# Kernel tuning notes

Measured on AMD Instinct MI355X. Metric: run time of the kernel, lower is better.

Reference implementation:

```python
import jax, jax.numpy as jnp
import numpy as np

H, W = 256, 256
L = 1024
R = 4
B = 64
EPS = 1e-4
FF = (H + W) * R * 4


def setup_inputs() -> dict:
    key = jax.random.key(0)
    ks = jax.random.split(key, 8)
    x = jax.random.normal(ks[0], (B, L), dtype=jnp.float32)
    # Linear weights (torch Linear: out = x @ W.T), kaiming-uniform-ish init
    lim = 1.0 / np.sqrt(L)
    W_t = jax.random.uniform(ks[1], (FF, L), minval=-lim, maxval=lim, dtype=jnp.float32)
    W_g = jax.random.uniform(ks[2], (FF, L), minval=-lim, maxval=lim, dtype=jnp.float32)
    # weights_static: [2, H, W, 2]
    k_lim = np.sqrt(6.0 / (H * W))
    ws0 = jax.random.uniform(ks[3], (1, H, W, 2), minval=-k_lim, maxval=k_lim, dtype=jnp.float32)
    ws1_re = jax.random.uniform(ks[4], (1, H, W, 1), minval=EPS - 1.0, maxval=1.0 - EPS, dtype=jnp.float32)
    ws1_im = jax.random.uniform(ks[5], (1, H, W, 1), minval=-EPS, maxval=EPS, dtype=jnp.float32)
    weights_static = jnp.concatenate([ws0, jnp.concatenate([ws1_re, ws1_im], axis=-1)], axis=0)
    x_lim = np.sqrt(6.0 / (H + W))
    weights_mod = jax.random.uniform(ks[6], (4, H, W), minval=-x_lim, maxval=x_lim, dtype=jnp.float32)
    c_lim = 1.0 / np.sqrt(R)
    kc1, kc2 = jax.random.split(ks[7])
    conv_w = jax.random.uniform(kc1, (R, R), minval=-c_lim, maxval=c_lim, dtype=jnp.float32)  # [out_ch, in_ch] for 1x1 conv
    conv_b = jax.random.uniform(kc2, (R,), minval=-c_lim, maxval=c_lim, dtype=jnp.float32)
    return {"x": x, "W_t": W_t, "W_g": W_g, "weights_static": weights_static,
            "weights_mod": weights_mod, "conv_w": conv_w, "conv_b": conv_b}


def reference(x, W_t, W_g, weights_static, weights_mod, conv_w, conv_b):
    b = x.shape[0]
    xt = x @ W_t.T                                  # [B, FF]
    xg = x @ W_g.T
    xg = xg * jax.nn.sigmoid(xg)                    # SiLU-style gate
    mod = xt * xg
    mod = mod.reshape(b, 4, -1)
    mod = mod / jnp.sqrt(jnp.mean(jnp.abs(mod), axis=-1, keepdims=True) + EPS)
    mod = mod.reshape(b, 4, R, H + W)
    a_part = mod[..., :H]                           # [B,4,R,H]
    b_part = mod[..., H:]                           # [B,4,R,W]
    outer = jnp.einsum('bkri,bkrj->bkrij', a_part, b_part)  # [B,4,R,H,W]
    # 1x1 conv (R->R) followed by sum over output channels collapses to a
    # single contraction with column-summed weights + summed bias (same math).
    w_eff = conv_w.sum(axis=0)                      # [R]
    b_eff = conv_b.sum()
    mod = jnp.einsum('bkrij,r->bkij', outer, w_eff) + b_eff  # [B,4,H,W]
    mod = weights_mod[None] * mod
    A0 = weights_static[0]                          # [H,W,2]
    A1 = weights_static[1]                          # [H,W,2]
    Bc = jnp.moveaxis(mod[:, 0:2], 1, -1)           # [B,H,W,2]
    re = A1[..., 0] * Bc[..., 0] - A1[..., 1] * Bc[..., 1]
    im = A1[..., 0] * Bc[..., 1] - A1[..., 1] * Bc[..., 0]
    mag = jnp.sqrt(re * re + im * im + EPS)         # [B,H,W]
    mag = jnp.sqrt(jnp.mean(mag, axis=(-1, -2)) + EPS)  # [B]
    inv = 1.0 / mag[:, None, None]
    mw_re = A0[..., 0] + re * inv                   # [B,H,W]
    mw_im = A0[..., 1] + im * inv
    proj = jnp.moveaxis(mod[:, 2:4], 1, -1)         # [B,H,W,2]
    den = jnp.sqrt(proj[..., 0] ** 2 + proj[..., 1] ** 2 + EPS)
    theta_cos = proj[..., 0] / den
    theta_sin = proj[..., 1] / den
    return mw_re * theta_cos + mw_im * theta_sin    # [B,H,W]
```

## Files before the change

kernel.cpp:

```cpp
#include <hip/hip_runtime.h>

typedef __bf16 bf16x8 __attribute__((ext_vector_type(8)));
typedef float floatx4 __attribute__((ext_vector_type(4)));

__device__ inline void cvt8_hl(const float* __restrict__ p, bf16x8& h, bf16x8& l){
  float4 v0 = *reinterpret_cast<const float4*>(p);
  float4 v1 = *reinterpret_cast<const float4*>(p + 4);
  float v[8] = {v0.x, v0.y, v0.z, v0.w, v1.x, v1.y, v1.z, v1.w};
  #pragma unroll
  for (int i = 0; i < 8; ++i) {
    __bf16 hi = (__bf16)v[i];
    h[i] = hi;
    l[i] = (__bf16)(v[i] - (float)hi);
  }
}

__global__ __launch_bounds__(256) void k1_gemm(
    const float* __restrict__ x,
    const float* __restrict__ Wt,
    const float* __restrict__ Wg,
    float* __restrict__ mod)
{
  __shared__ float red[3][32][64];
  const int tid  = threadIdx.x;
  const int wave = tid >> 6, lane = tid & 63;
  const int quad = lane >> 4, r16 = lane & 15;
  const int ff = blockIdx.x * 16 + r16;
  const int kb = wave * 256 + quad * 8;

  floatx4 accT[4], accG[4];
  #pragma unroll
  for (int m = 0; m < 4; ++m) { accT[m] = (floatx4)0.0f; accG[m] = (floatx4)0.0f; }

  const float* wt = Wt + ff * 1024 + kb;
  const float* wg = Wg + ff * 1024 + kb;
  const float* xp = x  + r16 * 1024 + kb;

  #pragma unroll
  for (int it = 0; it < 8; ++it) {
    const int ko = it * 32;
    bf16x8 bth, btl, bgh, bgl;
    cvt8_hl(wt + ko, bth, btl);
    cvt8_hl(wg + ko, bgh, bgl);
    #pragma unroll
    for (int mt = 0; mt < 4; ++mt) {
      bf16x8 ah, al;
      cvt8_hl(xp + mt * 16384 + ko, ah, al);
      accT[mt] = __builtin_amdgcn_mfma_f32_16x16x32_bf16(ah, bth, accT[mt], 0, 0, 0);
      accT[mt] = __builtin_amdgcn_mfma_f32_16x16x32_bf16(ah, btl, accT[mt], 0, 0, 0);
      accT[mt] = __builtin_amdgcn_mfma_f32_16x16x32_bf16(al, bth, accT[mt], 0, 0, 0);
      accG[mt] = __builtin_amdgcn_mfma_f32_16x16x32_bf16(ah, bgh, accG[mt], 0, 0, 0);
      accG[mt] = __builtin_amdgcn_mfma_f32_16x16x32_bf16(ah, bgl, accG[mt], 0, 0, 0);
      accG[mt] = __builtin_amdgcn_mfma_f32_16x16x32_bf16(al, bgh, accG[mt], 0, 0, 0);
    }
  }

  if (wave != 0) {
    #pragma unroll
    for (int mt = 0; mt < 4; ++mt)
      #pragma unroll
      for (int r = 0; r < 4; ++r) {
        red[wave - 1][mt * 4 + r][lane]      = accT[mt][r];
        red[wave - 1][16 + mt * 4 + r][lane] = accG[mt][r];
      }
  }
  __syncthreads();
  if (wave == 0) {
    #pragma unroll
    for (int mt = 0; mt < 4; ++mt) {
      #pragma unroll
      for (int r = 0; r < 4; ++r) {
        float t = accT[mt][r] + red[0][mt * 4 + r][lane]
                              + red[1][mt * 4 + r][lane]
                              + red[2][mt * 4 + r][lane];
        float g = accG[mt][r] + red[0][16 + mt * 4 + r][lane]
                              + red[1][16 + mt * 4 + r][lane]
                              + red[2][16 + mt * 4 + r][lane];
        float sig = 1.0f / (1.0f + __expf(-g));
        int b = mt * 16 + quad * 4 + r;
        mod[b * 8192 + ff] = t * g * sig;
      }
    }
  }
}

__global__ __launch_bounds__(256) void k1b_scale(const float* __restrict__ mod,
                                                 float* __restrict__ s)
{
  const int row = blockIdx.x;
  const int tid = threadIdx.x;
  const float* p = mod + row * 2048;
  float sum = 0.0f;
  #pragma unroll
  for (int q = 0; q < 8; ++q) sum += fabsf(p[q * 256 + tid]);
  #pragma unroll
  for (int o = 1; o < 64; o <<= 1) sum += __shfl_xor(sum, o, 64);
  __shared__ float ls[4];
  if ((tid & 63) == 0) ls[tid >> 6] = sum;
  __syncthreads();
  if (tid == 0) {
    float t = ls[0] + ls[1] + ls[2] + ls[3];
    s[row] = rsqrtf(t * (1.0f / 2048.0f) + 1e-4f);
  }
}

__global__ __launch_bounds__(256) void k2_mag(
    const float* __restrict__ mod, const float* __restrict__ s,
    const float* __restrict__ wstat,
    const float* __restrict__ wmod,
    const float* __restrict__ cw,
    const float* __restrict__ cb,
    float* __restrict__ partial)
{
  const int b = blockIdx.x, jc = blockIdx.y;
  const int tid = threadIdx.x;
  __shared__ __align__(16) float a_l[256 * 8];

  float weff[4]; float beff = 0.0f;
  #pragma unroll
  for (int r = 0; r < 4; ++r) {
    weff[r] = cw[r] + cw[4 + r] + cw[8 + r] + cw[12 + r];
    beff += cb[r];
  }
  const float s0 = s[b * 4 + 0], s1 = s[b * 4 + 1];
  const float* mb = mod + b * 8192;

  #pragma unroll
  for (int p = 0; p < 8; ++p) {
    int k = p >> 2, r = p & 3;
    float sc = (k ? s1 : s0) * weff[r];
    a_l[tid * 8 + p] = mb[k * 2048 + r * 512 + tid] * sc;
  }
  const int j = jc * 32 + (tid & 31);
  float bp[8];
  #pragma unroll
  for (int p = 0; p < 8; ++p) {
    int k = p >> 2, r = p & 3;
    bp[p] = mb[k * 2048 + r * 512 + 256 + j] * (k ? s1 : s0);
  }
  __syncthreads();

  const int ioff = tid >> 5;
  float acc = 0.0f;
  for (int it = 0; it < 32; ++it) {
    const int i = it * 8 + ioff;
    const float4 av0 = *reinterpret_cast<const float4*>(&a_l[i * 8]);
    const float4 av1 = *reinterpret_cast<const float4*>(&a_l[i * 8 + 4]);
    float d0 = av0.x * bp[0] + av0.y * bp[1] + av0.z * bp[2] + av0.w * bp[3];
    float d1 = av1.x * bp[4] + av1.y * bp[5] + av1.z * bp[6] + av1.w * bp[7];
    const int ij = i * 256 + j;
    float m0 = wmod[ij] * (d0 + beff);
    float m1 = wmod[65536 + ij] * (d1 + beff);
    float2 a1 = *reinterpret_cast<const float2*>(wstat + 131072 + ij * 2);
    float re = a1.x * m0 - a1.y * m1;
    float im = a1.x * m1 - a1.y * m0;
    acc += sqrtf(re * re + im * im + 1e-4f);
  }
  #pragma unroll
  for (int o = 1; o < 64; o <<= 1) acc += __shfl_xor(acc, o, 64);
  __shared__ float wsum[4];
  if ((tid & 63) == 0) wsum[tid >> 6] = acc;
  __syncthreads();
  if (tid == 0) partial[b * 8 + jc] = wsum[0] + wsum[1] + wsum[2] + wsum[3];
}

__global__ __launch_bounds__(256) void k4_out(
    const float* __restrict__ mod, const float* __restrict__ s,
    const float* __restrict__ wstat,
    const float* __restrict__ wmod,
    const float* __restrict__ cw,
    const float* __restrict__ cb,
    const float* __restrict__ partial,
    float* __restrict__ out)
{
  const int b = blockIdx.x, ibase = blockIdx.y * 32;
  const int tid = threadIdx.x;
  __shared__ __align__(16) float a_l[32 * 16];

  float weff[4]; float beff = 0.0f;
  #pragma unroll
  for (int r = 0; r < 4; ++r) {
    weff[r] = cw[r] + cw[4 + r] + cw[8 + r] + cw[12 + r];
    beff += cb[r];
  }
  float sk[4];
  #pragma unroll
  for (int k = 0; k < 4; ++k) sk[k] = s[b * 4 + k];
  const float* mb = mod + b * 8192;

  float tot = 0.0f;
  #pragma unroll
  for (int t = 0; t < 8; ++t) tot += partial[b * 8 + t];
  const float inv = rsqrtf(tot * (1.0f / 65536.0f) + 1e-4f);

  #pragma unroll
  for (int p = 0; p < 2; ++p) {
    int idx = p * 256 + tid;
    int il = idx & 31, kr = idx >> 5;
    int k = kr >> 2, r = kr & 3;
    a_l[il * 16 + kr] = mb[k * 2048 + r * 512 + ibase + il] * (sk[k] * weff[r]);
  }
  const int j = (tid & 127) * 2;
  const int ioff = tid >> 7;
  float bp0[16], bp1[16];
  #pragma unroll
  for (int kr = 0; kr < 16; ++kr) {
    int k = kr >> 2, r = kr & 3;
    float2 v = *reinterpret_cast<const float2*>(mb + k * 2048 + r * 512 + 256 + j);
    bp0[kr] = v.x * sk[k]; bp1[kr] = v.y * sk[k];
  }
  __syncthreads();

  #pragma unroll 2
  for (int it = 0; it < 16; ++it) {
    const int il = it * 2 + ioff;
    const int i = ibase + il;
    const float4 a0 = *reinterpret_cast<const float4*>(&a_l[il * 16]);
    const float4 a1 = *reinterpret_cast<const float4*>(&a_l[il * 16 + 4]);
    const float4 a2 = *reinterpret_cast<const float4*>(&a_l[il * 16 + 8]);
    const float4 a3 = *reinterpret_cast<const float4*>(&a_l[il * 16 + 12]);
    const int ij = i * 256 + j;
    const float2 wm0 = *reinterpret_cast<const float2*>(wmod + ij);
    const float2 wm1 = *reinterpret_cast<const float2*>(wmod + 65536 + ij);
    const float2 wm2 = *reinterpret_cast<const float2*>(wmod + 131072 + ij);
    const float2 wm3 = *reinterpret_cast<const float2*>(wmod + 196608 + ij);
    const float4 A0v = *reinterpret_cast<const float4*>(wstat + ij * 2);
    const float4 A1v = *reinterpret_cast<const float4*>(wstat + 131072 + ij * 2);
    float outv[2];
    #pragma unroll
    for (int e = 0; e < 2; ++e) {
      const float* bp = e ? bp1 : bp0;
      float d0 = a0.x * bp[0] + a0.y * bp[1] + a0.z * bp[2] + a0.w * bp[3];
      float d1 = a1.x * bp[4] + a1.y * bp[5] + a1.z * bp[6] + a1.w * bp[7];
      float d2 = a2.x * bp[8] + a2.y * bp[9] + a2.z * bp[10] + a2.w * bp[11];
      float d3 = a3.x * bp[12] + a3.y * bp[13] + a3.z * bp[14] + a3.w * bp[15];
      float m0 = (e ? wm0.y : wm0.x) * (d0 + beff);
      float m1 = (e ? wm1.y : wm1.x) * (d1 + beff);
      float m2 = (e ? wm2.y : wm2.x) * (d2 + beff);
      float m3 = (e ? wm3.y : wm3.x) * (d3 + beff);
      float A0r = e ? A0v.z : A0v.x;
      float A0i = e ? A0v.w : A0v.y;
      float A1r = e ? A1v.z : A1v.x;
      float A1i = e ? A1v.w : A1v.y;
      float re = A1r * m0 - A1i * m1;
      float im = A1r * m1 - A1i * m0;
      float mwre = A0r + re * inv;
      float mwim = A0i + im * inv;
      float rd = rsqrtf(m2 * m2 + m3 * m3 + 1e-4f);
      outv[e] = (mwre * m2 + mwim * m3) * rd;
    }
    *reinterpret_cast<float2*>(out + b * 65536 + ij) = make_float2(outv[0], outv[1]);
  }
}

extern "C" void kernel_launch(void* const* d_in, const int* in_sizes, int n_in,
                              void* d_out, int out_size, void* d_ws, size_t ws_size,
                              hipStream_t stream) {
  const float* x     = (const float*)d_in[0];
  const float* Wt    = (const float*)d_in[1];
  const float* Wg    = (const float*)d_in[2];
  const float* wstat = (const float*)d_in[3];
  const float* wmod  = (const float*)d_in[4];
  const float* cw    = (const float*)d_in[5];
  const float* cb    = (const float*)d_in[6];

  float* mod     = (float*)d_ws;
  float* sbuf    = mod + 524288;
  float* partial = sbuf + 256;

  k1_gemm  <<<512, 256, 0, stream>>>(x, Wt, Wg, mod);
  k1b_scale<<<256, 256, 0, stream>>>(mod, sbuf);
  k2_mag   <<<dim3(64, 8), 256, 0, stream>>>(mod, sbuf, wstat, wmod, cw, cb, partial);
  k4_out   <<<dim3(64, 8), 256, 0, stream>>>(mod, sbuf, wstat, wmod, cw, cb, partial,
                                             (float*)d_out);
}
```

Measured before the change: 152.2 us.

## Split GEMM K dimension across two blocks and prefetch weight registers

The GEMM grid gains a second dimension that splits the K reduction in half, doubling block count to fill more CUs, and weight loads are issued up front into registers before the MFMA loop. Partial T/G results are written to scratch and a new combine kernel sums the halves, applies the SiLU gate, and produces per-chunk abs sums. The scale kernel then reduces those partials in a single block instead of rereading mod. This adds an extra kernel launch and extra global traffic for the partial buffers.

```diff
diff --git a/kernel.cpp b/kernel.cpp
--- a/kernel.cpp
+++ b/kernel.cpp
@@ -3,9 +3,7 @@
 typedef __bf16 bf16x8 __attribute__((ext_vector_type(8)));
 typedef float floatx4 __attribute__((ext_vector_type(4)));
 
-__device__ inline void cvt8_hl(const float* __restrict__ p, bf16x8& h, bf16x8& l){
-  float4 v0 = *reinterpret_cast<const float4*>(p);
-  float4 v1 = *reinterpret_cast<const float4*>(p + 4);
+__device__ inline void cvt8_hl_r(float4 v0, float4 v1, bf16x8& h, bf16x8& l){
   float v[8] = {v0.x, v0.y, v0.z, v0.w, v1.x, v1.y, v1.z, v1.w};
   #pragma unroll
   for (int i = 0; i < 8; ++i) {
@@ -14,19 +12,23 @@
     l[i] = (__bf16)(v[i] - (float)hi);
   }
 }
+__device__ inline void cvt8_hl(const float* __restrict__ p, bf16x8& h, bf16x8& l){
+  cvt8_hl_r(*reinterpret_cast<const float4*>(p),
+            *reinterpret_cast<const float4*>(p + 4), h, l);
+}
 
 __global__ __launch_bounds__(256) void k1_gemm(
     const float* __restrict__ x,
     const float* __restrict__ Wt,
     const float* __restrict__ Wg,
-    float* __restrict__ mod)
+    float* __restrict__ pT, float* __restrict__ pG)
 {
   __shared__ float red[3][32][64];
   const int tid  = threadIdx.x;
   const int wave = tid >> 6, lane = tid & 63;
   const int quad = lane >> 4, r16 = lane & 15;
   const int ff = blockIdx.x * 16 + r16;
-  const int kb = wave * 256 + quad * 8;
+  const int kb = blockIdx.y * 512 + wave * 128 + quad * 8;
 
   floatx4 accT[4], accG[4];
   #pragma unroll
@@ -36,16 +38,24 @@
   const float* wg = Wg + ff * 1024 + kb;
   const float* xp = x  + r16 * 1024 + kb;
 
-  #pragma unroll
-  for (int it = 0; it < 8; ++it) {
-    const int ko = it * 32;
+  float4 wtv[8], wgv[8];
+  #pragma unroll
+  for (int it = 0; it < 4; ++it) {
+    wtv[it * 2]     = *reinterpret_cast<const float4*>(wt + it * 32);
+    wtv[it * 2 + 1] = *reinterpret_cast<const float4*>(wt + it * 32 + 4);
+    wgv[it * 2]     = *reinterpret_cast<const float4*>(wg + it * 32);
+    wgv[it * 2 + 1] = *reinterpret_cast<const float4*>(wg + it * 32 + 4);
+  }
+
+  #pragma unroll
+  for (int it = 0; it < 4; ++it) {
     bf16x8 bth, btl, bgh, bgl;
-    cvt8_hl(wt + ko, bth, btl);
-    cvt8_hl(wg + ko, bgh, bgl);
+    cvt8_hl_r(wtv[it * 2], wtv[it * 2 + 1], bth, btl);
+    cvt8_hl_r(wgv[it * 2], wgv[it * 2 + 1], bgh, bgl);
     #pragma unroll
     for (int mt = 0; mt < 4; ++mt) {
       bf16x8 ah, al;
-      cvt8_hl(xp + mt * 16384 + ko, ah, al);
+      cvt8_hl(xp + mt * 16384 + it * 32, ah, al);
       accT[mt] = __builtin_amdgcn_mfma_f32_16x16x32_bf16(ah, bth, accT[mt], 0, 0, 0);
       accT[mt] = __builtin_amdgcn_mfma_f32_16x16x32_bf16(ah, btl, accT[mt], 0, 0, 0);
       accT[mt] = __builtin_amdgcn_mfma_f32_16x16x32_bf16(al, bth, accT[mt], 0, 0, 0);
@@ -66,6 +76,7 @@
   }
   __syncthreads();
   if (wave == 0) {
+    const int base = blockIdx.y * 524288;
     #pragma unroll
     for (int mt = 0; mt < 4; ++mt) {
       #pragma unroll
@@ -76,32 +87,41 @@
         float g = accG[mt][r] + red[0][16 + mt * 4 + r][lane]
                               + red[1][16 + mt * 4 + r][lane]
                               + red[2][16 + mt * 4 + r][lane];
-        float sig = 1.0f / (1.0f + __expf(-g));
         int b = mt * 16 + quad * 4 + r;
-        mod[b * 8192 + ff] = t * g * sig;
+        pT[base + b * 8192 + ff] = t;
+        pG[base + b * 8192 + ff] = g;
       }
     }
   }
 }
 
-__global__ __launch_bounds__(256) void k1b_scale(const float* __restrict__ mod,
+__global__ __launch_bounds__(256) void k1c_combine(
+    const float* __restrict__ pT, const float* __restrict__ pG,
+    float* __restrict__ mod, float* __restrict__ part2)
+{
+  const int tid = threadIdx.x;
+  const int g = blockIdx.x * 256 + tid;
+  float t  = pT[g] + pT[g + 524288];
+  float gg = pG[g] + pG[g + 524288];
+  float m = t * gg / (1.0f + __expf(-gg));
+  mod[g] = m;
+  float a = fabsf(m);
+  #pragma unroll
+  for (int o = 1; o < 64; o <<= 1) a += __shfl_xor(a, o, 64);
+  __shared__ float ws[4];
+  if ((tid & 63) == 0) ws[tid >> 6] = a;
+  __syncthreads();
+  if (tid == 0) part2[blockIdx.x] = ws[0] + ws[1] + ws[2] + ws[3];
+}
+
+__global__ __launch_bounds__(256) void k1b_scale(const float* __restrict__ part2,
                                                  float* __restrict__ s)
 {
-  const int row = blockIdx.x;
-  const int tid = threadIdx.x;
-  const float* p = mod + row * 2048;
-  float sum = 0.0f;
-  #pragma unroll
-  for (int q = 0; q < 8; ++q) sum += fabsf(p[q * 256 + tid]);
-  #pragma unroll
-  for (int o = 1; o < 64; o <<= 1) sum += __shfl_xor(sum, o, 64);
-  __shared__ float ls[4];
-  if ((tid & 63) == 0) ls[tid >> 6] = sum;
-  __syncthreads();
-  if (tid == 0) {
-    float t = ls[0] + ls[1] + ls[2] + ls[3];
-    s[row] = rsqrtf(t * (1.0f / 2048.0f) + 1e-4f);
-  }
+  const int row = threadIdx.x;
+  float t = 0.0f;
+  #pragma unroll
+  for (int c = 0; c < 8; ++c) t += part2[row * 8 + c];
+  s[row] = rsqrtf(t * (1.0f / 2048.0f) + 1e-4f);
 }
 
 __global__ __launch_bounds__(256) void k2_mag(
@@ -264,13 +284,17 @@
   const float* cw    = (const float*)d_in[5];
   const float* cb    = (const float*)d_in[6];
 
-  float* mod     = (float*)d_ws;
-  float* sbuf    = mod + 524288;
+  float* pT      = (float*)d_ws;
+  float* pG      = pT + 1048576;
+  float* mod     = pG + 1048576;
+  float* part2   = mod + 524288;
+  float* sbuf    = part2 + 2048;
   float* partial = sbuf + 256;
 
-  k1_gemm  <<<512, 256, 0, stream>>>(x, Wt, Wg, mod);
-  k1b_scale<<<256, 256, 0, stream>>>(mod, sbuf);
-  k2_mag   <<<dim3(64, 8), 256, 0, stream>>>(mod, sbuf, wstat, wmod, cw, cb, partial);
-  k4_out   <<<dim3(64, 8), 256, 0, stream>>>(mod, sbuf, wstat, wmod, cw, cb, partial,
-                                             (float*)d_out);
-}
+  k1_gemm    <<<dim3(512, 2), 256, 0, stream>>>(x, Wt, Wg, pT, pG);
+  k1c_combine<<<2048, 256, 0, stream>>>(pT, pG, mod, part2);
+  k1b_scale  <<<1, 256, 0, stream>>>(part2, sbuf);
+  k2_mag     <<<dim3(64, 8), 256, 0, stream>>>(mod, sbuf, wstat, wmod, cw, cb, partial);
+  k4_out     <<<dim3(64, 8), 256, 0, stream>>>(mod, sbuf, wstat, wmod, cw, cb, partial,
+                                               (float*)d_out);
+}
```

Result: slower. 167.1 us (+9.8%).

## Split GEMM waves over batch tiles and double-buffer register loads

Applied to the files above, without the earlier changes.

The GEMM kernel previously split the K dimension across four waves, each computing all 64 batch rows, then reduced the partial sums through shared memory. Now each wave owns one 16-row batch tile and walks the full K range, so the shared-memory reduction and the barrier go away. Loads of the next K-slice are prefetched into registers while the current slice is converted and fed to MFMA. Each wave now re-reads the same weight rows, so weight traffic per block grows fourfold (likely served from cache), and each wave runs a longer serial chain of dependent MFMAs on only two accumulators.

```diff
diff --git a/kernel.cpp b/kernel.cpp
--- a/kernel.cpp
+++ b/kernel.cpp
@@ -3,9 +3,7 @@
 typedef __bf16 bf16x8 __attribute__((ext_vector_type(8)));
 typedef float floatx4 __attribute__((ext_vector_type(4)));
 
-__device__ inline void cvt8_hl(const float* __restrict__ p, bf16x8& h, bf16x8& l){
-  float4 v0 = *reinterpret_cast<const float4*>(p);
-  float4 v1 = *reinterpret_cast<const float4*>(p + 4);
+__device__ inline void cvt8_hl_r(float4 v0, float4 v1, bf16x8& h, bf16x8& l){
   float v[8] = {v0.x, v0.y, v0.z, v0.w, v1.x, v1.y, v1.z, v1.w};
   #pragma unroll
   for (int i = 0; i < 8; ++i) {
@@ -21,66 +19,60 @@
     const float* __restrict__ Wg,
     float* __restrict__ mod)
 {
-  __shared__ float red[3][32][64];
   const int tid  = threadIdx.x;
   const int wave = tid >> 6, lane = tid & 63;
   const int quad = lane >> 4, r16 = lane & 15;
   const int ff = blockIdx.x * 16 + r16;
-  const int kb = wave * 256 + quad * 8;
-
-  floatx4 accT[4], accG[4];
-  #pragma unroll
-  for (int m = 0; m < 4; ++m) { accT[m] = (floatx4)0.0f; accG[m] = (floatx4)0.0f; }
-
-  const float* wt = Wt + ff * 1024 + kb;
-  const float* wg = Wg + ff * 1024 + kb;
-  const float* xp = x  + r16 * 1024 + kb;
-
-  #pragma unroll
-  for (int it = 0; it < 8; ++it) {
-    const int ko = it * 32;
-    bf16x8 bth, btl, bgh, bgl;
-    cvt8_hl(wt + ko, bth, btl);
-    cvt8_hl(wg + ko, bgh, bgl);
-    #pragma unroll
-    for (int mt = 0; mt < 4; ++mt) {
-      bf16x8 ah, al;
-      cvt8_hl(xp + mt * 16384 + ko, ah, al);
-      accT[mt] = __builtin_amdgcn_mfma_f32_16x16x32_bf16(ah, bth, accT[mt], 0, 0, 0);
-      accT[mt] = __builtin_amdgcn_mfma_f32_16x16x32_bf16(ah, btl, accT[mt], 0, 0, 0);
-      accT[mt] = __builtin_amdgcn_mfma_f32_16x16x32_bf16(al, bth, accT[mt], 0, 0, 0);
-      accG[mt] = __builtin_amdgcn_mfma_f32_16x16x32_bf16(ah, bgh, accG[mt], 0, 0, 0);
-      accG[mt] = __builtin_amdgcn_mfma_f32_16x16x32_bf16(ah, bgl, accG[mt], 0, 0, 0);
-      accG[mt] = __builtin_amdgcn_mfma_f32_16x16x32_bf16(al, bgh, accG[mt], 0, 0, 0);
+  const int kq = quad * 8;
+
+  floatx4 accT[1], accG[1];
+  accT[0] = (floatx4)0.0f; accG[0] = (floatx4)0.0f;
+  floatx4 aT = (floatx4)0.0f, aG = (floatx4)0.0f;
+
+  const float* wt = Wt + ff * 1024 + kq;
+  const float* wg = Wg + ff * 1024 + kq;
+  const float* xp = x  + (wave * 16 + r16) * 1024 + kq;
+
+  float4 wtv[2][2], wgv[2][2], xv[2][2];
+  wtv[0][0] = *reinterpret_cast<const float4*>(wt);
+  wtv[0][1] = *reinterpret_cast<const float4*>(wt + 4);
+  wgv[0][0] = *reinterpret_cast<const float4*>(wg);
+  wgv[0][1] = *reinterpret_cast<const float4*>(wg + 4);
+  xv [0][0] = *reinterpret_cast<const float4*>(xp);
+  xv [0][1] = *reinterpret_cast<const float4*>(xp + 4);
+
+  #pragma unroll 4
+  for (int it = 0; it < 32; ++it) {
+    const int cur = it & 1, nxt = cur ^ 1;
+    if (it < 31) {
+      const int ko = (it + 1) * 32;
+      wtv[nxt][0] = *reinterpret_cast<const float4*>(wt + ko);
+      wtv[nxt][1] = *reinterpret_cast<const float4*>(wt + ko + 4);
+      wgv[nxt][0] = *reinterpret_cast<const float4*>(wg + ko);
+      wgv[nxt][1] = *reinterpret_cast<const float4*>(wg + ko + 4);
+      xv [nxt][0] = *reinterpret_cast<const float4*>(xp + ko);
+      xv [nxt][1] = *reinterpret_cast<const float4*>(xp + ko + 4);
     }
-  }
-
-  if (wave != 0) {
-    #pragma unroll
-    for (int mt = 0; mt < 4; ++mt)
-      #pragma unroll
-      for (int r = 0; r < 4; ++r) {
-        red[wave - 1][mt * 4 + r][lane]      = accT[mt][r];
-        red[wave - 1][16 + mt * 4 + r][lane] = accG[mt][r];
-      }
-  }
-  __syncthreads();
-  if (wave == 0) {
-    #pragma unroll
-    for (int mt = 0; mt < 4; ++mt) {
-      #pragma unroll
-      for (int r = 0; r < 4; ++r) {
-        float t = accT[mt][r] + red[0][mt * 4 + r][lane]
-                              + red[1][mt * 4 + r][lane]
-                              + red[2][mt * 4 + r][lane];
-        float g = accG[mt][r] + red[0][16 + mt * 4 + r][lane]
-                              + red[1][16 + mt * 4 + r][lane]
-                              + red[2][16 + mt * 4 + r][lane];
-        float sig = 1.0f / (1.0f + __expf(-g));
-        int b = mt * 16 + quad * 4 + r;
-        mod[b * 8192 + ff] = t * g * sig;
-      }
-    }
+    bf16x8 bth, btl, bgh, bgl, ah, al;
+    cvt8_hl_r(wtv[cur][0], wtv[cur][1], bth, btl);
+    cvt8_hl_r(wgv[cur][0], wgv[cur][1], bgh, bgl);
+    cvt8_hl_r(xv [cur][0], xv [cur][1], ah,  al);
+    aT = __builtin_amdgcn_mfma_f32_16x16x32_bf16(ah, bth, aT, 0, 0, 0);
+    aT = __builtin_amdgcn_mfma_f32_16x16x32_bf16(ah, btl, aT, 0, 0, 0);
+    aT = __builtin_amdgcn_mfma_f32_16x16x32_bf16(al, bth, aT, 0, 0, 0);
+    aG = __builtin_amdgcn_mfma_f32_16x16x32_bf16(ah, bgh, aG, 0, 0, 0);
+    aG = __builtin_amdgcn_mfma_f32_16x16x32_bf16(ah, bgl, aG, 0, 0, 0);
+    aG = __builtin_amdgcn_mfma_f32_16x16x32_bf16(al, bgh, aG, 0, 0, 0);
+  }
+  accT[0] = aT; accG[0] = aG;
+
+  #pragma unroll
+  for (int r = 0; r < 4; ++r) {
+    float t = accT[0][r];
+    float g = accG[0][r];
+    float sig = 1.0f / (1.0f + __expf(-g));
+    int b = wave * 16 + quad * 4 + r;
+    mod[b * 8192 + ff] = t * g * sig;
   }
 }
 
```

New measurement: 171.2 us. +12.5%, slower.
